# Performance work log

Measured on AMD Instinct MI355X. Metric: run time of the kernel, lower is better.

## Reference

```python
import jax, jax.numpy as jnp
import numpy as np

GEN_POLY = ("1011011", "1111001")  # constraint_length 7, rate 1/2
LARGE = 1e9  # metric for infeasible start states


def _build_trellis(gen_poly):
    """Static trellis tables (numpy, built at trace time).

    State = last mu input bits (most recent bit is MSB), matching the
    shift-register convention: next_state = [u, s_bits[:-1]].
    """
    conv_n = len(gen_poly)
    K = len(gen_poly[0])
    mu = K - 1
    ns, ni, no = 2 ** mu, 2, 2 ** conv_n
    g = np.array([[int(c) for c in p] for p in gen_poly])  # (conv_n, K)
    to_nodes = np.zeros((ns, ni), np.int32)
    op = np.zeros((ns, ni), np.int32)
    for s in range(ns):
        s_bits = [(s >> (mu - 1 - i)) & 1 for i in range(mu)]
        for u in range(ni):
            reg = np.array([u] + s_bits)          # [u_t, u_{t-1}, ..., u_{t-mu}]
            outs = (g @ reg) % 2                  # conv_n output bits
            op[s, u] = int("".join(map(str, outs)), 2)
            to_nodes[s, u] = int("".join(map(str, [u] + s_bits[:-1])), 2)
    from_nodes = np.zeros((ns, ni), np.int32)
    op_by_tonode = np.zeros((ns, ni), np.int32)
    cnt = np.zeros(ns, np.int32)
    for s in range(ns):
        for u in range(ni):
            t = to_nodes[s, u]
            from_nodes[t, cnt[t]] = s
            op_by_tonode[t, cnt[t]] = op[s, u]
            cnt[t] += 1
    op_bits = np.array([[(o >> (conv_n - 1 - j)) & 1 for j in range(conv_n)]
                        for o in range(no)], np.float32)  # (no, conv_n)
    return conv_n, ns, ni, to_nodes, from_nodes, op_by_tonode, op_bits


def setup_inputs() -> dict:
    key = jax.random.key(0)
    # noisy channel LLRs for B=512 codewords of length n=4096
    inputs = jax.random.normal(key, (512, 4096), dtype=jnp.float32) * 2.0
    return {"inputs": inputs}


def reference(inputs):
    conv_n, ns, ni, to_nodes_np, from_nodes_np, op_by_tonode_np, op_bits = \
        _build_trellis(GEN_POLY)
    tn = jnp.asarray(to_nodes_np)       # (ns, ni) next state
    fn = jnp.asarray(from_nodes_np)     # (ns, ni) predecessor states
    opt = jnp.asarray(op_by_tonode_np)  # (ns, ni) output symbol on that branch

    B, n = inputs.shape
    T = n // conv_n                     # number of trellis steps / info bits
    y = inputs.reshape(B, T, conv_n)

    # soft_llr branch metrics: bm[t,b,o] = sum_c y[b,t,c] * (1 - 2*op_bit[o,c])
    sign = jnp.asarray(1.0 - 2.0 * op_bits)          # (no, conv_n)
    bm = jnp.einsum('btc,oc->tbo', y, sign)          # (T, B, no)

    cum0 = jnp.full((B, ns), LARGE, jnp.float32).at[:, 0].set(0.0)
    st_rng = jnp.arange(ns)

    def acs(cum, bm_t):
        # add: metric of (prev_state i, output symbol j)
        sm = bm_t[:, None, :] + cum[:, :, None]      # (B, ns, no)
        # gather by to-node: candidates for each next state
        cand = sm[:, fn, opt]                        # (B, ns, ni)
        j = jnp.argmin(cand, axis=2)                 # compare-select
        tb = fn[st_rng[None, :], j]                  # traceback predecessor (B, ns)
        cum_t = jnp.min(cand, axis=2)
        return cum_t, (cum_t, tb)

    cum_T, (cms, tbs) = jax.lax.scan(acs, cum0, bm)  # tbs: (T, B, ns)

    # traceback from optimal terminal state
    term = jnp.argmin(cum_T, axis=1).astype(jnp.int32)

    def tb_step(st, tb_t):
        prev = jnp.take_along_axis(tb_t, st[:, None], axis=1)[:, 0]
        return prev, st

    p0, ys = jax.lax.scan(tb_step, term, tbs[1:], reverse=True)
    # path states at times 0..T (initial state is 0)
    paths = jnp.concatenate(
        [jnp.zeros((B, 1), jnp.int32), p0[:, None], jnp.swapaxes(ys, 0, 1)],
        axis=1)                                       # (B, T+1)

    # recover input bit per transition: bit u s.t. to_nodes[prev, u] == next
    match = tn[paths[:, :-1]] == paths[:, 1:][:, :, None]  # (B, T, ni)
    bits = jnp.sum(jnp.where(match, jnp.arange(ni, dtype=jnp.int32), 0), axis=-1)
    return bits.astype(jnp.float32)                   # (B, T) hard bit estimates
```

## Files before the change

kernel.cpp:

```cpp
#include <hip/hip_runtime.h>
#include <stdint.h>

#define T_STEPS 2048
#define NCHUNK  86
#define LARGEF  1.0e9f
typedef unsigned long long u64;
typedef unsigned uint2v __attribute__((ext_vector_type(2)));

__device__ __forceinline__ int par6(int x) { return __builtin_popcount((unsigned)x) & 1; }

constexpr int CARR[6] = {5, 6, 12, 8, 16, 32};

template<int CTRL>
__device__ __forceinline__ float xdpp(float x) {
  return __int_as_float(__builtin_amdgcn_update_dpp(0, __float_as_int(x), CTRL, 0xF, 0xF, true));
}
template<int CTRL>
__device__ __forceinline__ unsigned xdpp_u(unsigned x) {
  return (unsigned)__builtin_amdgcn_update_dpp(0, (int)x, CTRL, 0xF, 0xF, true);
}

__device__ __forceinline__ unsigned selmask_u(unsigned a_false, unsigned b_true, u64 m) {
  unsigned out;
  asm("v_cndmask_b32 %0, %1, %2, %3" : "=v"(out) : "v"(a_false), "v"(b_true), "s"(m));
  return out;
}

__device__ __forceinline__ unsigned exch16_u(unsigned x, u64 mrx) {
#if __has_builtin(__builtin_amdgcn_permlane16_swap)
  uint2v r = __builtin_amdgcn_permlane16_swap(x, x, false, false);
  return selmask_u(r.y, r.x, mrx);
#else
  (void)mrx;
  return (unsigned)__builtin_amdgcn_ds_swizzle((int)x, 0x401F);
#endif
}
__device__ __forceinline__ unsigned exch32_u(unsigned x, u64 mrx) {
#if __has_builtin(__builtin_amdgcn_permlane32_swap)
  uint2v r = __builtin_amdgcn_permlane32_swap(x, x, false, false);
  return selmask_u(r.y, r.x, mrx);
#else
  (void)mrx;
  return (unsigned)__shfl_xor((int)x, 32, 64);
#endif
}
__device__ __forceinline__ float exch16_f(float x, u64 mrx) {
  return __uint_as_float(exch16_u(__float_as_uint(x), mrx));
}
__device__ __forceinline__ float exch32_f(float x, u64 mrx) {
  return __uint_as_float(exch32_u(__float_as_uint(x), mrx));
}

struct Ctx {
  float sae[6], sbe[6];
  unsigned pdu[6];
  u64 pdm[6];
  u64 mrx16, mrx32;
};

template<int N>
__device__ __forceinline__ void bmcalc(const float4 (&fy)[12], float (&bm)[24], const Ctx& cx) {
#pragma unroll
  for (int k = 0; k < N; ++k) {
    const int ph = k % 6;
    const float y0 = (k & 1) ? fy[k >> 1].z : fy[k >> 1].x;
    const float y1 = (k & 1) ? fy[k >> 1].w : fy[k >> 1].y;
    bm[k] = fmaf(cx.sae[ph], y0, cx.sbe[ph] * y1);
  }
}

template<int N, int K>
__device__ __forceinline__ void fsteps(float& cum, unsigned& word,
                                       const float (&bm)[24], const Ctx& cx) {
  if constexpr (K < N) {
    constexpr int ph = K % 6;
    float ex; unsigned exw;
    if constexpr (ph == 0)      { ex = xdpp<0xB1>(cum);  exw = xdpp_u<0xB1>(word); }
    else if constexpr (ph == 1) { ex = xdpp<0x4E>(cum);  exw = xdpp_u<0x4E>(word); }
    else if constexpr (ph == 2) { ex = xdpp<0x141>(cum); exw = xdpp_u<0x141>(word); }
    else if constexpr (ph == 3) { ex = xdpp<0x140>(cum); exw = xdpp_u<0x140>(word); }
    else if constexpr (ph == 4) { ex = exch16_f(cum, cx.mrx16); exw = exch16_u(word, cx.mrx16); }
    else                        { ex = exch32_f(cum, cx.mrx32); exw = exch32_u(word, cx.mrx32); }
    const float cA = cum + bm[K];
    const float cB = ex - bm[K];
    const u64 b1 = __ballot(cB < cA);
    const u64 b2 = __ballot(cA < cB);
    const u64 tpm = (b1 & ~cx.pdm[ph]) | (cx.pdm[ph] & ~b2);
    word = selmask_u(word, exw, tpm) | (cx.pdu[ph] << (6 + K));
    cum = fminf(cA, cB);
    fsteps<N, K + 1>(cum, word, bm, cx);
  }
}

__global__ __launch_bounds__(64, 1) void viterbi_kernel(const float* __restrict__ in,
                                                        float* __restrict__ out) {
  __shared__ float y_lds[2 * T_STEPS];
  __shared__ unsigned tbf[NCHUNK * 64];

  const int b = blockIdx.x;
  const int lane = threadIdx.x;
  const float* yrow = in + (size_t)b * (2 * T_STEPS);

  {
    const float4* g = (const float4*)yrow;
    float4* l = (float4*)y_lds;
#pragma unroll
    for (int i = 0; i < 16; ++i) l[i * 64 + lane] = g[i * 64 + lane];
  }
  __syncthreads();

  Ctx cx;
#pragma unroll
  for (int ph = 0; ph < 6; ++ph) {
    const int pdv = par6(lane & CARR[ph]);
    int t = 0;
#pragma unroll
    for (int j = 0; j < 5; ++j) t |= par6(lane & CARR[(ph + 1 + j) % 6]) << j;
    t |= pdv << 5;
    const float sa = 1.0f - 2.0f * (float)par6(t & 45);
    const float sb = 1.0f - 2.0f * (float)par6(t & 60);
    cx.sae[ph] = pdv ? -sa : sa;
    cx.sbe[ph] = pdv ? -sb : sb;
    cx.pdu[ph] = (unsigned)pdv;
    cx.pdm[ph] = __ballot(pdv != 0);
  }
  {
    const u64 ODD16 = 0xFFFF0000FFFF0000ull;
    const u64 HI32  = 0xFFFFFFFF00000000ull;
#if __has_builtin(__builtin_amdgcn_permlane16_swap)
    uint2v p16 = __builtin_amdgcn_permlane16_swap((unsigned)lane, (unsigned)lane, false, false);
    const bool rxo = ((unsigned)__builtin_amdgcn_readlane((int)p16.x, 0) == 16u);
    cx.mrx16 = rxo ? ~ODD16 : ODD16;
#else
    cx.mrx16 = 0;
#endif
#if __has_builtin(__builtin_amdgcn_permlane32_swap)
    uint2v p32 = __builtin_amdgcn_permlane32_swap((unsigned)lane, (unsigned)lane, false, false);
    const bool rxh = ((unsigned)__builtin_amdgcn_readlane((int)p32.x, 0) == 32u);
    cx.mrx32 = rxh ? ~HI32 : HI32;
#else
    cx.mrx32 = 0;
#endif
  }

  float cum = (lane == 0) ? 0.0f : LARGEF;
  unsigned word = (unsigned)lane;
  float bm[24];
  float4 cur[12], nxt[12];
  const float4* y4 = (const float4*)y_lds;
#pragma unroll
  for (int j = 0; j < 12; ++j) cur[j] = y4[j];
  for (int cc = 0; cc < 42; ++cc) {
    const int c0 = 2 * cc;
    bmcalc<24>(cur, bm, cx);
#pragma unroll
    for (int j = 0; j < 12; ++j) nxt[j] = y4[12 * (c0 + 1) + j];
    fsteps<24, 0>(cum, word, bm, cx);
    tbf[c0 * 64 + lane] = word; word = (unsigned)lane;
    bmcalc<24>(nxt, bm, cx);
#pragma unroll
    for (int j = 0; j < 12; ++j) cur[j] = y4[12 * (c0 + 2) + j];
    fsteps<24, 0>(cum, word, bm, cx);
    tbf[(c0 + 1) * 64 + lane] = word; word = (unsigned)lane;
  }
  bmcalc<24>(cur, bm, cx);
#pragma unroll
  for (int j = 0; j < 4; ++j) nxt[j] = y4[1020 + j];
  fsteps<24, 0>(cum, word, bm, cx);
  tbf[84 * 64 + lane] = word; word = (unsigned)lane;
  bmcalc<8>(nxt, bm, cx);
  fsteps<8, 0>(cum, word, bm, cx);
  tbf[85 * 64 + lane] = word;

  const int stf = par6(lane & 12) | (par6(lane & 8) << 1) | (par6(lane & 16) << 2) |
                  (par6(lane & 32) << 3) | (par6(lane & 5) << 4) | (par6(lane & 6) << 5);
  float v = cum; int bs = stf; int bl = lane;
#pragma unroll
  for (int off = 32; off >= 1; off >>= 1) {
    const float ov = __shfl_xor(v, off, 64);
    const int os = __shfl_xor(bs, off, 64);
    const int ol = __shfl_xor(bl, off, 64);
    if (ov < v || (ov == v && os < bs)) { v = ov; bs = os; bl = ol; }
  }
  int lam = __builtin_amdgcn_readfirstlane(bl);

  const size_t ob = (size_t)b * T_STEPS;
  unsigned row = tbf[85 * 64 + lane];
  for (int c = 85; c >= 0; --c) {
    unsigned nrow = 0;
    if (c > 0) nrow = tbf[(c - 1) * 64 + lane];
    const unsigned w = (unsigned)__builtin_amdgcn_readlane((int)row, lam);
    const int nb = (c == 85) ? 8 : 24;
    if (lane < nb) out[ob + c * 24 + lane] = (float)((w >> (6 + lane)) & 1u);
    lam = (int)(w & 63u);
    row = nrow;
  }
}

extern "C" void kernel_launch(void* const* d_in, const int* in_sizes, int n_in,
                              void* d_out, int out_size, void* d_ws, size_t ws_size,
                              hipStream_t stream) {
  const float* in = (const float*)d_in[0];
  float* out = (float*)d_out;
  (void)in_sizes; (void)n_in; (void)out_size; (void)d_ws; (void)ws_size;
  viterbi_kernel<<<dim3(512), dim3(64), 0, stream>>>(in, out);
}
```

Before: 74.79 us.

## Fuse pairs of Viterbi ACS steps into radix-4 rounds with combined exchanges

Replaces the per-step radix-2 add-compare-select with a radix-4 round that processes two trellis steps at once. Each lane gathers three partner metrics (two single exchanges and one combined exchange) and computes the two-step minimum directly, so the second step no longer waits on the first step's exchange. This shortens the serial dependency chain per pair of steps. In return each round needs more exchange, ballot and select instructions and more precomputed sign/mask registers.

```diff
diff --git a/kernel.cpp b/kernel.cpp
--- a/kernel.cpp
+++ b/kernel.cpp
@@ -10,6 +10,7 @@
 __device__ __forceinline__ int par6(int x) { return __builtin_popcount((unsigned)x) & 1; }
 
 constexpr int CARR[6] = {5, 6, 12, 8, 16, 32};
+constexpr int MARR[6] = {1, 2, 7, 15, 16, 32};
 
 template<int CTRL>
 __device__ __forceinline__ float xdpp(float x) {
@@ -52,43 +53,77 @@
 }
 
 struct Ctx {
-  float sae[6], sbe[6];
-  unsigned pdu[6];
-  u64 pdm[6];
+  float saeA[3], sbeA[3];
+  float saeA2[3], sbeA2[3];
+  float saeB[3], sbeB[3];
+  unsigned pq0[3], pq1[3];
+  u64 pdmA[3], pdmA2[3], pdmB[3];
   u64 mrx16, mrx32;
 };
 
-template<int N>
-__device__ __forceinline__ void bmcalc(const float4 (&fy)[12], float (&bm)[24], const Ctx& cx) {
-#pragma unroll
-  for (int k = 0; k < N; ++k) {
-    const int ph = k % 6;
-    const float y0 = (k & 1) ? fy[k >> 1].z : fy[k >> 1].x;
-    const float y1 = (k & 1) ? fy[k >> 1].w : fy[k >> 1].y;
-    bm[k] = fmaf(cx.sae[ph], y0, cx.sbe[ph] * y1);
-  }
-}
-
-template<int N, int K>
-__device__ __forceinline__ void fsteps(float& cum, unsigned& word,
-                                       const float (&bm)[24], const Ctx& cx) {
-  if constexpr (K < N) {
-    constexpr int ph = K % 6;
-    float ex; unsigned exw;
-    if constexpr (ph == 0)      { ex = xdpp<0xB1>(cum);  exw = xdpp_u<0xB1>(word); }
-    else if constexpr (ph == 1) { ex = xdpp<0x4E>(cum);  exw = xdpp_u<0x4E>(word); }
-    else if constexpr (ph == 2) { ex = xdpp<0x141>(cum); exw = xdpp_u<0x141>(word); }
-    else if constexpr (ph == 3) { ex = xdpp<0x140>(cum); exw = xdpp_u<0x140>(word); }
-    else if constexpr (ph == 4) { ex = exch16_f(cum, cx.mrx16); exw = exch16_u(word, cx.mrx16); }
-    else                        { ex = exch32_f(cum, cx.mrx32); exw = exch32_u(word, cx.mrx32); }
-    const float cA = cum + bm[K];
-    const float cB = ex - bm[K];
-    const u64 b1 = __ballot(cB < cA);
-    const u64 b2 = __ballot(cA < cB);
-    const u64 tpm = (b1 & ~cx.pdm[ph]) | (cx.pdm[ph] & ~b2);
-    word = selmask_u(word, exw, tpm) | (cx.pdu[ph] << (6 + K));
-    cum = fminf(cA, cB);
-    fsteps<N, K + 1>(cum, word, bm, cx);
+__device__ __forceinline__ void mk(int ph, int l, float& sae, float& sbe, int& pd) {
+  const int pdv = par6(l & CARR[ph]);
+  int t = 0;
+#pragma unroll
+  for (int j = 0; j < 5; ++j) t |= par6(l & CARR[(ph + 1 + j) % 6]) << j;
+  t |= pdv << 5;
+  const float sa = 1.0f - 2.0f * (float)par6(t & 45);
+  const float sb = 1.0f - 2.0f * (float)par6(t & 60);
+  sae = pdv ? -sa : sa;
+  sbe = pdv ? -sb : sb;
+  pd = pdv;
+}
+
+template<int NR>
+__device__ __forceinline__ void bmcalc3(const float4 (&fy)[12], float (&bmA)[12],
+                                        float (&bmA2)[12], float (&bmB)[12], const Ctx& cx) {
+#pragma unroll
+  for (int r = 0; r < NR; ++r) {
+    const int rp = r % 3;
+    bmA[r]  = fmaf(cx.saeA[rp],  fy[r].x, cx.sbeA[rp]  * fy[r].y);
+    bmA2[r] = fmaf(cx.saeA2[rp], fy[r].x, cx.sbeA2[rp] * fy[r].y);
+    bmB[r]  = fmaf(cx.saeB[rp],  fy[r].z, cx.sbeB[rp]  * fy[r].w);
+  }
+}
+
+template<int NR, int R>
+__device__ __forceinline__ void frounds(float& cum, unsigned& word,
+                                        const float (&bmA)[12], const float (&bmA2)[12],
+                                        const float (&bmB)[12], const Ctx& cx) {
+  if constexpr (R < NR) {
+    constexpr int RP = R % 3;
+    float exA, exB_, exAB; unsigned wxA, wxB, wxAB;
+    if constexpr (RP == 0) {
+      exA  = xdpp<0xB1>(cum);  exB_ = xdpp<0x4E>(cum);  exAB = xdpp<0x1B>(cum);
+      wxA  = xdpp_u<0xB1>(word); wxB = xdpp_u<0x4E>(word); wxAB = xdpp_u<0x1B>(word);
+    } else if constexpr (RP == 1) {
+      exA  = xdpp<0x141>(cum); exB_ = xdpp<0x140>(cum); exAB = xdpp<0x128>(cum);
+      wxA  = xdpp_u<0x141>(word); wxB = xdpp_u<0x140>(word); wxAB = xdpp_u<0x128>(word);
+    } else {
+      exA  = exch16_f(cum, cx.mrx16);  exB_ = exch32_f(cum, cx.mrx32);
+      exAB = exch16_f(exB_, cx.mrx16);
+      wxA  = exch16_u(word, cx.mrx16); wxB  = exch32_u(word, cx.mrx32);
+      wxAB = exch16_u(wxB, cx.mrx16);
+    }
+    const float c00p = cum  + bmA[R];
+    const float c01p = exA  - bmA[R];
+    const float c10p = exB_ + bmA2[R];
+    const float c11p = exAB - bmA2[R];
+    const float u = fminf(c00p, c01p);
+    const float v = fminf(c10p, c11p);
+    const float x  = u + bmB[R];
+    const float yv = v - bmB[R];
+    cum = fminf(x, yv);
+    const u64 a1 = __ballot(c01p < c00p), a2 = __ballot(c00p < c01p);
+    const u64 o1 = __ballot(c11p < c10p), o2 = __ballot(c10p < c11p);
+    const u64 f1 = __ballot(yv < x),      f2 = __ballot(x < yv);
+    const u64 dA  = (a1 & ~cx.pdmA[RP])  | (cx.pdmA[RP]  & ~a2);
+    const u64 dAo = (o1 & ~cx.pdmA2[RP]) | (cx.pdmA2[RP] & ~o2);
+    const u64 dB  = (f1 & ~cx.pdmB[RP])  | (cx.pdmB[RP]  & ~f2);
+    const unsigned wu = selmask_u(word, wxA, dA)  | (cx.pq0[RP] << (6 + 2 * R));
+    const unsigned wv = selmask_u(wxB, wxAB, dAo) | (cx.pq1[RP] << (6 + 2 * R));
+    word = selmask_u(wu, wv, dB);
+    frounds<NR, R + 1>(cum, word, bmA, bmA2, bmB, cx);
   }
 }
 
@@ -111,18 +146,18 @@
 
   Ctx cx;
 #pragma unroll
-  for (int ph = 0; ph < 6; ++ph) {
-    const int pdv = par6(lane & CARR[ph]);
-    int t = 0;
-#pragma unroll
-    for (int j = 0; j < 5; ++j) t |= par6(lane & CARR[(ph + 1 + j) % 6]) << j;
-    t |= pdv << 5;
-    const float sa = 1.0f - 2.0f * (float)par6(t & 45);
-    const float sb = 1.0f - 2.0f * (float)par6(t & 60);
-    cx.sae[ph] = pdv ? -sa : sa;
-    cx.sbe[ph] = pdv ? -sb : sb;
-    cx.pdu[ph] = (unsigned)pdv;
-    cx.pdm[ph] = __ballot(pdv != 0);
+  for (int rp = 0; rp < 3; ++rp) {
+    const int pA = 2 * rp, pB = 2 * rp + 1;
+    const int mB = MARR[pB];
+    float sa, sb; int pd;
+    mk(pA, lane, sa, sb, pd);        cx.saeA[rp] = sa;  cx.sbeA[rp] = sb;  const int pdA = pd;
+    mk(pA, lane ^ mB, sa, sb, pd);   cx.saeA2[rp] = sa; cx.sbeA2[rp] = sb; const int pdA2 = pd;
+    mk(pB, lane, sa, sb, pd);        cx.saeB[rp] = sa;  cx.sbeB[rp] = sb;  const int pdB = pd;
+    cx.pq0[rp] = (unsigned)(pdA  | (pdB << 1));
+    cx.pq1[rp] = (unsigned)(pdA2 | (pdB << 1));
+    cx.pdmA[rp]  = __ballot(pdA != 0);
+    cx.pdmA2[rp] = __ballot(pdA2 != 0);
+    cx.pdmB[rp]  = __ballot(pdB != 0);
   }
   {
     const u64 ODD16 = 0xFFFF0000FFFF0000ull;
@@ -145,31 +180,31 @@
 
   float cum = (lane == 0) ? 0.0f : LARGEF;
   unsigned word = (unsigned)lane;
-  float bm[24];
+  float bmA[12], bmA2[12], bmB[12];
   float4 cur[12], nxt[12];
   const float4* y4 = (const float4*)y_lds;
 #pragma unroll
   for (int j = 0; j < 12; ++j) cur[j] = y4[j];
   for (int cc = 0; cc < 42; ++cc) {
     const int c0 = 2 * cc;
-    bmcalc<24>(cur, bm, cx);
+    bmcalc3<12>(cur, bmA, bmA2, bmB, cx);
 #pragma unroll
     for (int j = 0; j < 12; ++j) nxt[j] = y4[12 * (c0 + 1) + j];
-    fsteps<24, 0>(cum, word, bm, cx);
+    frounds<12, 0>(cum, word, bmA, bmA2, bmB, cx);
     tbf[c0 * 64 + lane] = word; word = (unsigned)lane;
-    bmcalc<24>(nxt, bm, cx);
+    bmcalc3<12>(nxt, bmA, bmA2, bmB, cx);
 #pragma unroll
     for (int j = 0; j < 12; ++j) cur[j] = y4[12 * (c0 + 2) + j];
-    fsteps<24, 0>(cum, word, bm, cx);
+    frounds<12, 0>(cum, word, bmA, bmA2, bmB, cx);
     tbf[(c0 + 1) * 64 + lane] = word; word = (unsigned)lane;
   }
-  bmcalc<24>(cur, bm, cx);
+  bmcalc3<12>(cur, bmA, bmA2, bmB, cx);
 #pragma unroll
   for (int j = 0; j < 4; ++j) nxt[j] = y4[1020 + j];
-  fsteps<24, 0>(cum, word, bm, cx);
+  frounds<12, 0>(cum, word, bmA, bmA2, bmB, cx);
   tbf[84 * 64 + lane] = word; word = (unsigned)lane;
-  bmcalc<8>(nxt, bm, cx);
-  fsteps<8, 0>(cum, word, bm, cx);
+  bmcalc3<4>(nxt, bmA, bmA2, bmB, cx);
+  frounds<4, 0>(cum, word, bmA, bmA2, bmB, cx);
   tbf[85 * 64 + lane] = word;
 
   const int stf = par6(lane & 12) | (par6(lane & 8) << 1) | (par6(lane & 16) << 2) |
```

After: 105.1 us. +40.6%, slower.

## Split Viterbi into ACS wave and helper wave for branch metrics and traceback words

Applied to the files above, without the earlier changes.

The block grows to two wavefronts. Wave 0 runs only the add-compare-select recursion and records one decision bit per step via an inline-asm xor/cmp/addc sequence. Wave 1 precomputes branch metrics into a triple-buffered LDS ring and rebuilds the survivor traceback words from those decision bits one chunk behind. This shortens the serial critical path of the ACS wave by moving the metric FMAs, word exchanges and selects off it. In exchange it adds a block-wide barrier every chunk (about 86 in total) and extra LDS traffic, and the barrier cost could offset the shorter per-step chain.

```diff
diff --git a/kernel.cpp b/kernel.cpp
--- a/kernel.cpp
+++ b/kernel.cpp
@@ -19,13 +19,11 @@
 __device__ __forceinline__ unsigned xdpp_u(unsigned x) {
   return (unsigned)__builtin_amdgcn_update_dpp(0, (int)x, CTRL, 0xF, 0xF, true);
 }
-
 __device__ __forceinline__ unsigned selmask_u(unsigned a_false, unsigned b_true, u64 m) {
   unsigned out;
   asm("v_cndmask_b32 %0, %1, %2, %3" : "=v"(out) : "v"(a_false), "v"(b_true), "s"(m));
   return out;
 }
-
 __device__ __forceinline__ unsigned exch16_u(unsigned x, u64 mrx) {
 #if __has_builtin(__builtin_amdgcn_permlane16_swap)
   uint2v r = __builtin_amdgcn_permlane16_swap(x, x, false, false);
@@ -44,72 +42,113 @@
   return (unsigned)__shfl_xor((int)x, 32, 64);
 #endif
 }
-__device__ __forceinline__ float exch16_f(float x, u64 mrx) {
-  return __uint_as_float(exch16_u(__float_as_uint(x), mrx));
-}
-__device__ __forceinline__ float exch32_f(float x, u64 mrx) {
-  return __uint_as_float(exch32_u(__float_as_uint(x), mrx));
-}
-
-struct Ctx {
-  float sae[6], sbe[6];
-  unsigned pdu[6];
-  u64 pdm[6];
-  u64 mrx16, mrx32;
-};
-
-template<int N>
-__device__ __forceinline__ void bmcalc(const float4 (&fy)[12], float (&bm)[24], const Ctx& cx) {
-#pragma unroll
-  for (int k = 0; k < N; ++k) {
-    const int ph = k % 6;
-    const float y0 = (k & 1) ? fy[k >> 1].z : fy[k >> 1].x;
-    const float y1 = (k & 1) ? fy[k >> 1].w : fy[k >> 1].y;
-    bm[k] = fmaf(cx.sae[ph], y0, cx.sbe[ph] * y1);
-  }
+template<int PH>
+__device__ __forceinline__ float exchf(float x, const u64 (&mrx)[2]) {
+  if constexpr (PH == 0) return xdpp<0xB1>(x);
+  else if constexpr (PH == 1) return xdpp<0x4E>(x);
+  else if constexpr (PH == 2) return xdpp<0x141>(x);
+  else if constexpr (PH == 3) return xdpp<0x140>(x);
+  else if constexpr (PH == 4) return __uint_as_float(exch16_u(__float_as_uint(x), mrx[0]));
+  else return __uint_as_float(exch32_u(__float_as_uint(x), mrx[1]));
+}
+template<int PH>
+__device__ __forceinline__ unsigned exchu(unsigned x, const u64 (&mrx)[2]) {
+  if constexpr (PH == 0) return xdpp_u<0xB1>(x);
+  else if constexpr (PH == 1) return xdpp_u<0x4E>(x);
+  else if constexpr (PH == 2) return xdpp_u<0x141>(x);
+  else if constexpr (PH == 3) return xdpp_u<0x140>(x);
+  else if constexpr (PH == 4) return exch16_u(x, mrx[0]);
+  else return exch32_u(x, mrx[1]);
+}
+
+template<int K>
+__device__ __forceinline__ float getbm(const float4 (&bk)[6]) {
+  constexpr int j = K >> 2;
+  if constexpr ((K & 3) == 0) return bk[j].x;
+  else if constexpr ((K & 3) == 1) return bk[j].y;
+  else if constexpr ((K & 3) == 2) return bk[j].z;
+  else return bk[j].w;
 }
 
 template<int N, int K>
-__device__ __forceinline__ void fsteps(float& cum, unsigned& word,
-                                       const float (&bm)[24], const Ctx& cx) {
+__device__ __forceinline__ void acsr(float& cum, unsigned& dw, const float4 (&bk)[6],
+                                     const unsigned (&sgn)[6], const u64 (&mrx)[2]) {
   if constexpr (K < N) {
     constexpr int ph = K % 6;
-    float ex; unsigned exw;
-    if constexpr (ph == 0)      { ex = xdpp<0xB1>(cum);  exw = xdpp_u<0xB1>(word); }
-    else if constexpr (ph == 1) { ex = xdpp<0x4E>(cum);  exw = xdpp_u<0x4E>(word); }
-    else if constexpr (ph == 2) { ex = xdpp<0x141>(cum); exw = xdpp_u<0x141>(word); }
-    else if constexpr (ph == 3) { ex = xdpp<0x140>(cum); exw = xdpp_u<0x140>(word); }
-    else if constexpr (ph == 4) { ex = exch16_f(cum, cx.mrx16); exw = exch16_u(word, cx.mrx16); }
-    else                        { ex = exch32_f(cum, cx.mrx32); exw = exch32_u(word, cx.mrx32); }
-    const float cA = cum + bm[K];
-    const float cB = ex - bm[K];
-    const u64 b1 = __ballot(cB < cA);
-    const u64 b2 = __ballot(cA < cB);
-    const u64 tpm = (b1 & ~cx.pdm[ph]) | (cx.pdm[ph] & ~b2);
-    word = selmask_u(word, exw, tpm) | (cx.pdu[ph] << (6 + K));
+    const float bmk = getbm<K>(bk);
+    const float ex = exchf<ph>(cum, mrx);
+    const float cA = cum + bmk;
+    const float cB = ex - bmk;
+    const float D = cA - cB;
     cum = fminf(cA, cB);
-    fsteps<N, K + 1>(cum, word, bm, cx);
-  }
-}
-
-__global__ __launch_bounds__(64, 1) void viterbi_kernel(const float* __restrict__ in,
-                                                        float* __restrict__ out) {
+    unsigned tmp;
+    asm("v_xor_b32 %0, %2, %3\n\t"
+        "v_cmp_gt_f32 vcc, 0, %0\n\t"
+        "v_addc_co_u32 %1, vcc, %1, %1, vcc"
+        : "=&v"(tmp), "+v"(dw)
+        : "v"(D), "v"(sgn[ph]) : "vcc");
+    acsr<N, K + 1>(cum, dw, bk, sgn, mrx);
+  }
+}
+
+template<int N, int K>
+__device__ __forceinline__ void wrec(unsigned& word, unsigned& dws, const unsigned (&pdu)[6],
+                                     const u64 (&pdm)[6], const u64 (&mrx)[2]) {
+  if constexpr (K < N) {
+    constexpr int ph = K % 6;
+    const unsigned exw = exchu<ph>(word, mrx);
+    asm("v_cmp_gt_i32 vcc, 0, %1\n\t"
+        "v_add_u32 %1, %1, %1\n\t"
+        "s_xor_b64 vcc, vcc, %3\n\t"
+        "v_cndmask_b32 %0, %0, %2, vcc"
+        : "+v"(word), "+v"(dws)
+        : "v"(exw), "s"(pdm[ph]) : "vcc");
+    word |= pdu[ph] << (6 + K);
+    wrec<N, K + 1>(word, dws, pdu, pdm, mrx);
+  }
+}
+
+template<int N>
+__device__ __forceinline__ void bmw(const float* ych, float* dst,
+                                    const float (&sae)[6], const float (&sbe)[6]) {
+  const float4* y4 = (const float4*)ych;
+  float4* d4 = (float4*)dst;
+#pragma unroll
+  for (int j = 0; j < N / 4; ++j) {
+    const float4 qa = y4[2 * j];
+    const float4 qb = y4[2 * j + 1];
+    float4 r;
+    r.x = fmaf(sae[(4 * j + 0) % 6], qa.x, sbe[(4 * j + 0) % 6] * qa.y);
+    r.y = fmaf(sae[(4 * j + 1) % 6], qa.z, sbe[(4 * j + 1) % 6] * qa.w);
+    r.z = fmaf(sae[(4 * j + 2) % 6], qb.x, sbe[(4 * j + 2) % 6] * qb.y);
+    r.w = fmaf(sae[(4 * j + 3) % 6], qb.z, sbe[(4 * j + 3) % 6] * qb.w);
+    d4[j] = r;
+  }
+}
+
+__global__ __launch_bounds__(128, 1) void viterbi_kernel(const float* __restrict__ in,
+                                                         float* __restrict__ out) {
   __shared__ float y_lds[2 * T_STEPS];
-  __shared__ unsigned tbf[NCHUNK * 64];
-
+  __shared__ float bmld[3][64][24];
+  __shared__ unsigned dwld[2][64];
+  __shared__ unsigned tbf[NCHUNK][64];
+  __shared__ int lam_sh;
+
+  const int tid = threadIdx.x;
+  const int lane = tid & 63;
+  const int w = tid >> 6;
   const int b = blockIdx.x;
-  const int lane = threadIdx.x;
-  const float* yrow = in + (size_t)b * (2 * T_STEPS);
 
   {
-    const float4* g = (const float4*)yrow;
+    const float4* g = (const float4*)(in + (size_t)b * (2 * T_STEPS));
     float4* l = (float4*)y_lds;
 #pragma unroll
-    for (int i = 0; i < 16; ++i) l[i * 64 + lane] = g[i * 64 + lane];
-  }
-  __syncthreads();
-
-  Ctx cx;
+    for (int i = 0; i < 8; ++i) l[i * 128 + tid] = g[i * 128 + tid];
+  }
+
+  float sae[6], sbe[6];
+  unsigned pdu[6], sgn[6];
+  u64 pdm[6], mrx[2];
 #pragma unroll
   for (int ph = 0; ph < 6; ++ph) {
     const int pdv = par6(lane & CARR[ph]);
@@ -119,81 +158,136 @@
     t |= pdv << 5;
     const float sa = 1.0f - 2.0f * (float)par6(t & 45);
     const float sb = 1.0f - 2.0f * (float)par6(t & 60);
-    cx.sae[ph] = pdv ? -sa : sa;
-    cx.sbe[ph] = pdv ? -sb : sb;
-    cx.pdu[ph] = (unsigned)pdv;
-    cx.pdm[ph] = __ballot(pdv != 0);
+    sae[ph] = pdv ? -sa : sa;
+    sbe[ph] = pdv ? -sb : sb;
+    pdu[ph] = (unsigned)pdv;
+    sgn[ph] = pdv ? 0u : 0x80000000u;
+    pdm[ph] = __ballot(pdv != 0);
   }
   {
     const u64 ODD16 = 0xFFFF0000FFFF0000ull;
-    const u64 HI32  = 0xFFFFFFFF00000000ull;
+    const u64 HI32 = 0xFFFFFFFF00000000ull;
 #if __has_builtin(__builtin_amdgcn_permlane16_swap)
     uint2v p16 = __builtin_amdgcn_permlane16_swap((unsigned)lane, (unsigned)lane, false, false);
-    const bool rxo = ((unsigned)__builtin_amdgcn_readlane((int)p16.x, 0) == 16u);
-    cx.mrx16 = rxo ? ~ODD16 : ODD16;
+    mrx[0] = (((unsigned)__builtin_amdgcn_readlane((int)p16.x, 0) == 16u)) ? ~ODD16 : ODD16;
 #else
-    cx.mrx16 = 0;
+    mrx[0] = 0;
 #endif
 #if __has_builtin(__builtin_amdgcn_permlane32_swap)
     uint2v p32 = __builtin_amdgcn_permlane32_swap((unsigned)lane, (unsigned)lane, false, false);
-    const bool rxh = ((unsigned)__builtin_amdgcn_readlane((int)p32.x, 0) == 32u);
-    cx.mrx32 = rxh ? ~HI32 : HI32;
+    mrx[1] = (((unsigned)__builtin_amdgcn_readlane((int)p32.x, 0) == 32u)) ? ~HI32 : HI32;
 #else
-    cx.mrx32 = 0;
+    mrx[1] = 0;
 #endif
   }
+  __syncthreads();
+
+  if (w == 1) {
+    bmw<24>(y_lds + 0, &bmld[0][lane][0], sae, sbe);
+    bmw<24>(y_lds + 48, &bmld[1][lane][0], sae, sbe);
+  }
+  __syncthreads();
 
   float cum = (lane == 0) ? 0.0f : LARGEF;
-  unsigned word = (unsigned)lane;
-  float bm[24];
-  float4 cur[12], nxt[12];
-  const float4* y4 = (const float4*)y_lds;
-#pragma unroll
-  for (int j = 0; j < 12; ++j) cur[j] = y4[j];
-  for (int cc = 0; cc < 42; ++cc) {
-    const int c0 = 2 * cc;
-    bmcalc<24>(cur, bm, cx);
-#pragma unroll
-    for (int j = 0; j < 12; ++j) nxt[j] = y4[12 * (c0 + 1) + j];
-    fsteps<24, 0>(cum, word, bm, cx);
-    tbf[c0 * 64 + lane] = word; word = (unsigned)lane;
-    bmcalc<24>(nxt, bm, cx);
-#pragma unroll
-    for (int j = 0; j < 12; ++j) cur[j] = y4[12 * (c0 + 2) + j];
-    fsteps<24, 0>(cum, word, bm, cx);
-    tbf[(c0 + 1) * 64 + lane] = word; word = (unsigned)lane;
-  }
-  bmcalc<24>(cur, bm, cx);
-#pragma unroll
-  for (int j = 0; j < 4; ++j) nxt[j] = y4[1020 + j];
-  fsteps<24, 0>(cum, word, bm, cx);
-  tbf[84 * 64 + lane] = word; word = (unsigned)lane;
-  bmcalc<8>(nxt, bm, cx);
-  fsteps<8, 0>(cum, word, bm, cx);
-  tbf[85 * 64 + lane] = word;
-
-  const int stf = par6(lane & 12) | (par6(lane & 8) << 1) | (par6(lane & 16) << 2) |
-                  (par6(lane & 32) << 3) | (par6(lane & 5) << 4) | (par6(lane & 6) << 5);
-  float v = cum; int bs = stf; int bl = lane;
-#pragma unroll
-  for (int off = 32; off >= 1; off >>= 1) {
-    const float ov = __shfl_xor(v, off, 64);
-    const int os = __shfl_xor(bs, off, 64);
-    const int ol = __shfl_xor(bl, off, 64);
-    if (ov < v || (ov == v && os < bs)) { v = ov; bs = os; bl = ol; }
-  }
-  int lam = __builtin_amdgcn_readfirstlane(bl);
-
-  const size_t ob = (size_t)b * T_STEPS;
-  unsigned row = tbf[85 * 64 + lane];
-  for (int c = 85; c >= 0; --c) {
-    unsigned nrow = 0;
-    if (c > 0) nrow = tbf[(c - 1) * 64 + lane];
-    const unsigned w = (unsigned)__builtin_amdgcn_readlane((int)row, lam);
-    const int nb = (c == 85) ? 8 : 24;
-    if (lane < nb) out[ob + c * 24 + lane] = (float)((w >> (6 + lane)) & 1u);
-    lam = (int)(w & 63u);
-    row = nrow;
+  unsigned dw = 0;
+  float4 bk0[6], bk1[6];
+  if (w == 0) {
+    const float4* p = (const float4*)&bmld[0][lane][0];
+#pragma unroll
+    for (int j = 0; j < 6; ++j) bk0[j] = p[j];
+  }
+
+#define W0_BLOCK(J)                                                                     \
+  {                                                                                     \
+    const float4* p = (const float4*)&bmld[((J) + 1) % 3][lane][0];                     \
+    if constexpr (((J) & 1) == 0) {                                                     \
+      _Pragma("unroll") for (int j = 0; j < 6; ++j) bk1[j] = p[j];                      \
+      acsr<24, 0>(cum, dw, bk0, sgn, mrx);                                              \
+    } else {                                                                            \
+      _Pragma("unroll") for (int j = 0; j < 6; ++j) bk0[j] = p[j];                      \
+      acsr<24, 0>(cum, dw, bk1, sgn, mrx);                                              \
+    }                                                                                   \
+    dwld[(J) & 1][lane] = dw;                                                           \
+    dw = 0;                                                                             \
+  }
+#define W1_BLOCK(J)                                                                     \
+  {                                                                                     \
+    const int c2 = base + (J) + 2;                                                      \
+    if (c2 != 85) bmw<24>(y_lds + 48 * c2, &bmld[((J) + 2) % 3][lane][0], sae, sbe);    \
+    else          bmw<8>(y_lds + 48 * c2, &bmld[((J) + 2) % 3][lane][0], sae, sbe);     \
+    if (base + (J) >= 1) {                                                              \
+      unsigned dws = dwld[((J) + 1) & 1][lane] << 8;                                    \
+      unsigned word = (unsigned)lane;                                                   \
+      wrec<24, 0>(word, dws, pdu, pdm, mrx);                                            \
+      tbf[base + (J) - 1][lane] = word;                                                 \
+    }                                                                                   \
+  }
+#define ITER(J)                                                                         \
+  if (w == 0) W0_BLOCK(J) else W1_BLOCK(J)                                              \
+  __syncthreads();
+
+  for (int base = 0; base < 84; base += 6) {
+    ITER(0) ITER(1) ITER(2) ITER(3) ITER(4) ITER(5)
+  }
+
+  if (w == 0) {
+    const float4* p = (const float4*)&bmld[1][lane][0];
+#pragma unroll
+    for (int j = 0; j < 6; ++j) bk1[j] = p[j];
+    acsr<24, 0>(cum, dw, bk0, sgn, mrx);
+    dwld[0][lane] = dw;
+    dw = 0;
+  } else {
+    unsigned dws = dwld[1][lane] << 8;
+    unsigned word = (unsigned)lane;
+    wrec<24, 0>(word, dws, pdu, pdm, mrx);
+    tbf[83][lane] = word;
+  }
+  __syncthreads();
+  if (w == 0) {
+    acsr<8, 0>(cum, dw, bk1, sgn, mrx);
+    dwld[1][lane] = dw;
+  } else {
+    unsigned dws = dwld[0][lane] << 8;
+    unsigned word = (unsigned)lane;
+    wrec<24, 0>(word, dws, pdu, pdm, mrx);
+    tbf[84][lane] = word;
+  }
+  __syncthreads();
+
+  if (w == 0) {
+    const int stf = par6(lane & 12) | (par6(lane & 8) << 1) | (par6(lane & 16) << 2) |
+                    (par6(lane & 32) << 3) | (par6(lane & 5) << 4) | (par6(lane & 6) << 5);
+    float v = cum; int bs = stf; int bl = lane;
+#pragma unroll
+    for (int off = 32; off >= 1; off >>= 1) {
+      const float ov = __shfl_xor(v, off, 64);
+      const int os = __shfl_xor(bs, off, 64);
+      const int ol = __shfl_xor(bl, off, 64);
+      if (ov < v || (ov == v && os < bs)) { v = ov; bs = os; bl = ol; }
+    }
+    if (lane == 0) lam_sh = bl;
+  } else {
+    unsigned dws = dwld[1][lane] << 24;
+    unsigned word = (unsigned)lane;
+    wrec<8, 0>(word, dws, pdu, pdm, mrx);
+    tbf[85][lane] = word;
+  }
+  __syncthreads();
+
+  if (w == 1) {
+    const size_t ob = (size_t)b * T_STEPS;
+    int lam = __builtin_amdgcn_readfirstlane(lam_sh);
+    unsigned row = tbf[85][lane];
+    for (int c = 85; c >= 0; --c) {
+      unsigned nrow = 0;
+      if (c > 0) nrow = tbf[c - 1][lane];
+      const unsigned ww = (unsigned)__builtin_amdgcn_readlane((int)row, lam);
+      const int nb = (c == 85) ? 8 : 24;
+      if (lane < nb) out[ob + c * 24 + lane] = (float)((ww >> (6 + lane)) & 1u);
+      lam = (int)(ww & 63u);
+      row = nrow;
+    }
   }
 }
 
@@ -203,5 +297,5 @@
   const float* in = (const float*)d_in[0];
   float* out = (float*)d_out;
   (void)in_sizes; (void)n_in; (void)out_size; (void)d_ws; (void)ws_size;
-  viterbi_kernel<<<dim3(512), dim3(64), 0, stream>>>(in, out);
-}
+  viterbi_kernel<<<dim3(512), dim3(128), 0, stream>>>(in, out);
+}
```

New measurement: 90.21 us. 20.6% more time.

## Split Viterbi into forward decision-bit pass, parallel chunk traceback rebuild, and traceback kernels

Applied to the files above, without the earlier changes.

The forward ACS loop now records one compare decision bit per step, produced with a compact xor/cmp/addc asm sequence. The per-step exchange and select of traceback words is removed from the serial critical path. A separate massively parallel kernel rebuilds the per-chunk traceback words from these decision bits, and a third kernel does the final traceback. This trades a shorter serial forward chain for extra global-memory round trips, two additional kernel launches, and workspace use, with a single fused fallback kernel when the workspace is too small.

```diff
diff --git a/kernel.cpp b/kernel.cpp
--- a/kernel.cpp
+++ b/kernel.cpp
@@ -4,6 +4,7 @@
 #define T_STEPS 2048
 #define NCHUNK  86
 #define LARGEF  1.0e9f
+#define NB      512
 typedef unsigned long long u64;
 typedef unsigned uint2v __attribute__((ext_vector_type(2)));
 
@@ -19,13 +20,11 @@
 __device__ __forceinline__ unsigned xdpp_u(unsigned x) {
   return (unsigned)__builtin_amdgcn_update_dpp(0, (int)x, CTRL, 0xF, 0xF, true);
 }
-
 __device__ __forceinline__ unsigned selmask_u(unsigned a_false, unsigned b_true, u64 m) {
   unsigned out;
   asm("v_cndmask_b32 %0, %1, %2, %3" : "=v"(out) : "v"(a_false), "v"(b_true), "s"(m));
   return out;
 }
-
 __device__ __forceinline__ unsigned exch16_u(unsigned x, u64 mrx) {
 #if __has_builtin(__builtin_amdgcn_permlane16_swap)
   uint2v r = __builtin_amdgcn_permlane16_swap(x, x, false, false);
@@ -44,134 +43,118 @@
   return (unsigned)__shfl_xor((int)x, 32, 64);
 #endif
 }
-__device__ __forceinline__ float exch16_f(float x, u64 mrx) {
-  return __uint_as_float(exch16_u(__float_as_uint(x), mrx));
-}
-__device__ __forceinline__ float exch32_f(float x, u64 mrx) {
-  return __uint_as_float(exch32_u(__float_as_uint(x), mrx));
-}
-
-struct Ctx {
+template<int PH>
+__device__ __forceinline__ float exchf(float x, const u64 (&mrx)[2]) {
+  if constexpr (PH == 0) return xdpp<0xB1>(x);
+  else if constexpr (PH == 1) return xdpp<0x4E>(x);
+  else if constexpr (PH == 2) return xdpp<0x141>(x);
+  else if constexpr (PH == 3) return xdpp<0x140>(x);
+  else if constexpr (PH == 4) return __uint_as_float(exch16_u(__float_as_uint(x), mrx[0]));
+  else return __uint_as_float(exch32_u(__float_as_uint(x), mrx[1]));
+}
+template<int PH>
+__device__ __forceinline__ unsigned exchu(unsigned x, const u64 (&mrx)[2]) {
+  if constexpr (PH == 0) return xdpp_u<0xB1>(x);
+  else if constexpr (PH == 1) return xdpp_u<0x4E>(x);
+  else if constexpr (PH == 2) return xdpp_u<0x141>(x);
+  else if constexpr (PH == 3) return xdpp_u<0x140>(x);
+  else if constexpr (PH == 4) return exch16_u(x, mrx[0]);
+  else return exch32_u(x, mrx[1]);
+}
+
+struct Phc {
   float sae[6], sbe[6];
+  unsigned sgn[6];
   unsigned pdu[6];
   u64 pdm[6];
-  u64 mrx16, mrx32;
+  u64 mrx[2];
 };
 
+__device__ __forceinline__ void mkconsts(int lane, Phc& p) {
+#pragma unroll
+  for (int ph = 0; ph < 6; ++ph) {
+    const int pdv = par6(lane & CARR[ph]);
+    int t = 0;
+#pragma unroll
+    for (int j = 0; j < 5; ++j) t |= par6(lane & CARR[(ph + 1 + j) % 6]) << j;
+    t |= pdv << 5;
+    const float sa = 1.0f - 2.0f * (float)par6(t & 45);
+    const float sb = 1.0f - 2.0f * (float)par6(t & 60);
+    p.sae[ph] = pdv ? -sa : sa;
+    p.sbe[ph] = pdv ? -sb : sb;
+    p.sgn[ph] = pdv ? 0u : 0x80000000u;
+    p.pdu[ph] = (unsigned)pdv;
+    p.pdm[ph] = __ballot(pdv != 0);
+  }
+  const u64 ODD16 = 0xFFFF0000FFFF0000ull, HI32 = 0xFFFFFFFF00000000ull;
+#if __has_builtin(__builtin_amdgcn_permlane16_swap)
+  {
+    uint2v r = __builtin_amdgcn_permlane16_swap((unsigned)lane, (unsigned)lane, false, false);
+    p.mrx[0] = (((unsigned)__builtin_amdgcn_readlane((int)r.x, 0) == 16u)) ? ~ODD16 : ODD16;
+  }
+#else
+  p.mrx[0] = 0;
+#endif
+#if __has_builtin(__builtin_amdgcn_permlane32_swap)
+  {
+    uint2v r = __builtin_amdgcn_permlane32_swap((unsigned)lane, (unsigned)lane, false, false);
+    p.mrx[1] = (((unsigned)__builtin_amdgcn_readlane((int)r.x, 0) == 32u)) ? ~HI32 : HI32;
+  }
+#else
+  p.mrx[1] = 0;
+#endif
+}
+
 template<int N>
-__device__ __forceinline__ void bmcalc(const float4 (&fy)[12], float (&bm)[24], const Ctx& cx) {
+__device__ __forceinline__ void bmcalc(const float4 (&fy)[12], float (&bm)[24],
+                                       const float (&sae)[6], const float (&sbe)[6]) {
 #pragma unroll
   for (int k = 0; k < N; ++k) {
     const int ph = k % 6;
     const float y0 = (k & 1) ? fy[k >> 1].z : fy[k >> 1].x;
     const float y1 = (k & 1) ? fy[k >> 1].w : fy[k >> 1].y;
-    bm[k] = fmaf(cx.sae[ph], y0, cx.sbe[ph] * y1);
+    bm[k] = fmaf(sae[ph], y0, sbe[ph] * y1);
   }
 }
 
 template<int N, int K>
-__device__ __forceinline__ void fsteps(float& cum, unsigned& word,
-                                       const float (&bm)[24], const Ctx& cx) {
+__device__ __forceinline__ void acs(float& cum, unsigned& dw, const float (&bm)[24],
+                                    const unsigned (&sgn)[6], const u64 (&mrx)[2]) {
   if constexpr (K < N) {
     constexpr int ph = K % 6;
-    float ex; unsigned exw;
-    if constexpr (ph == 0)      { ex = xdpp<0xB1>(cum);  exw = xdpp_u<0xB1>(word); }
-    else if constexpr (ph == 1) { ex = xdpp<0x4E>(cum);  exw = xdpp_u<0x4E>(word); }
-    else if constexpr (ph == 2) { ex = xdpp<0x141>(cum); exw = xdpp_u<0x141>(word); }
-    else if constexpr (ph == 3) { ex = xdpp<0x140>(cum); exw = xdpp_u<0x140>(word); }
-    else if constexpr (ph == 4) { ex = exch16_f(cum, cx.mrx16); exw = exch16_u(word, cx.mrx16); }
-    else                        { ex = exch32_f(cum, cx.mrx32); exw = exch32_u(word, cx.mrx32); }
+    const float ex = exchf<ph>(cum, mrx);
     const float cA = cum + bm[K];
     const float cB = ex - bm[K];
-    const u64 b1 = __ballot(cB < cA);
-    const u64 b2 = __ballot(cA < cB);
-    const u64 tpm = (b1 & ~cx.pdm[ph]) | (cx.pdm[ph] & ~b2);
-    word = selmask_u(word, exw, tpm) | (cx.pdu[ph] << (6 + K));
+    const float D = cA - cB;
     cum = fminf(cA, cB);
-    fsteps<N, K + 1>(cum, word, bm, cx);
-  }
-}
-
-__global__ __launch_bounds__(64, 1) void viterbi_kernel(const float* __restrict__ in,
-                                                        float* __restrict__ out) {
-  __shared__ float y_lds[2 * T_STEPS];
-  __shared__ unsigned tbf[NCHUNK * 64];
-
-  const int b = blockIdx.x;
-  const int lane = threadIdx.x;
-  const float* yrow = in + (size_t)b * (2 * T_STEPS);
-
-  {
-    const float4* g = (const float4*)yrow;
-    float4* l = (float4*)y_lds;
-#pragma unroll
-    for (int i = 0; i < 16; ++i) l[i * 64 + lane] = g[i * 64 + lane];
-  }
-  __syncthreads();
-
-  Ctx cx;
-#pragma unroll
-  for (int ph = 0; ph < 6; ++ph) {
-    const int pdv = par6(lane & CARR[ph]);
-    int t = 0;
-#pragma unroll
-    for (int j = 0; j < 5; ++j) t |= par6(lane & CARR[(ph + 1 + j) % 6]) << j;
-    t |= pdv << 5;
-    const float sa = 1.0f - 2.0f * (float)par6(t & 45);
-    const float sb = 1.0f - 2.0f * (float)par6(t & 60);
-    cx.sae[ph] = pdv ? -sa : sa;
-    cx.sbe[ph] = pdv ? -sb : sb;
-    cx.pdu[ph] = (unsigned)pdv;
-    cx.pdm[ph] = __ballot(pdv != 0);
-  }
-  {
-    const u64 ODD16 = 0xFFFF0000FFFF0000ull;
-    const u64 HI32  = 0xFFFFFFFF00000000ull;
-#if __has_builtin(__builtin_amdgcn_permlane16_swap)
-    uint2v p16 = __builtin_amdgcn_permlane16_swap((unsigned)lane, (unsigned)lane, false, false);
-    const bool rxo = ((unsigned)__builtin_amdgcn_readlane((int)p16.x, 0) == 16u);
-    cx.mrx16 = rxo ? ~ODD16 : ODD16;
-#else
-    cx.mrx16 = 0;
-#endif
-#if __has_builtin(__builtin_amdgcn_permlane32_swap)
-    uint2v p32 = __builtin_amdgcn_permlane32_swap((unsigned)lane, (unsigned)lane, false, false);
-    const bool rxh = ((unsigned)__builtin_amdgcn_readlane((int)p32.x, 0) == 32u);
-    cx.mrx32 = rxh ? ~HI32 : HI32;
-#else
-    cx.mrx32 = 0;
-#endif
-  }
-
-  float cum = (lane == 0) ? 0.0f : LARGEF;
-  unsigned word = (unsigned)lane;
-  float bm[24];
-  float4 cur[12], nxt[12];
-  const float4* y4 = (const float4*)y_lds;
-#pragma unroll
-  for (int j = 0; j < 12; ++j) cur[j] = y4[j];
-  for (int cc = 0; cc < 42; ++cc) {
-    const int c0 = 2 * cc;
-    bmcalc<24>(cur, bm, cx);
-#pragma unroll
-    for (int j = 0; j < 12; ++j) nxt[j] = y4[12 * (c0 + 1) + j];
-    fsteps<24, 0>(cum, word, bm, cx);
-    tbf[c0 * 64 + lane] = word; word = (unsigned)lane;
-    bmcalc<24>(nxt, bm, cx);
-#pragma unroll
-    for (int j = 0; j < 12; ++j) cur[j] = y4[12 * (c0 + 2) + j];
-    fsteps<24, 0>(cum, word, bm, cx);
-    tbf[(c0 + 1) * 64 + lane] = word; word = (unsigned)lane;
-  }
-  bmcalc<24>(cur, bm, cx);
-#pragma unroll
-  for (int j = 0; j < 4; ++j) nxt[j] = y4[1020 + j];
-  fsteps<24, 0>(cum, word, bm, cx);
-  tbf[84 * 64 + lane] = word; word = (unsigned)lane;
-  bmcalc<8>(nxt, bm, cx);
-  fsteps<8, 0>(cum, word, bm, cx);
-  tbf[85 * 64 + lane] = word;
-
+    unsigned tmp;
+    asm("v_xor_b32 %0, %2, %3\n\t"
+        "v_cmp_gt_f32 vcc, 0, %0\n\t"
+        "v_addc_co_u32 %1, vcc, %1, %1, vcc"
+        : "=&v"(tmp), "+v"(dw)
+        : "v"(D), "v"(sgn[ph]) : "vcc");
+    acs<N, K + 1>(cum, dw, bm, sgn, mrx);
+  }
+}
+
+template<int N, int K>
+__device__ __forceinline__ void wrec(unsigned& word, unsigned& dws, const unsigned (&pdu)[6],
+                                     const u64 (&pdm)[6], const u64 (&mrx)[2]) {
+  if constexpr (K < N) {
+    constexpr int ph = K % 6;
+    const unsigned exw = exchu<ph>(word, mrx);
+    asm("v_cmp_gt_i32 vcc, 0, %1\n\t"
+        "v_add_u32 %1, %1, %1\n\t"
+        "s_xor_b64 vcc, vcc, %3\n\t"
+        "v_cndmask_b32 %0, %0, %2, vcc"
+        : "+v"(word), "+v"(dws)
+        : "v"(exw), "s"(pdm[ph]) : "vcc");
+    word |= pdu[ph] << (6 + K);
+    wrec<N, K + 1>(word, dws, pdu, pdm, mrx);
+  }
+}
+
+__device__ __forceinline__ int term_argmin(float cum, int lane) {
   const int stf = par6(lane & 12) | (par6(lane & 8) << 1) | (par6(lane & 16) << 2) |
                   (par6(lane & 32) << 3) | (par6(lane & 5) << 4) | (par6(lane & 6) << 5);
   float v = cum; int bs = stf; int bl = lane;
@@ -182,13 +165,169 @@
     const int ol = __shfl_xor(bl, off, 64);
     if (ov < v || (ov == v && os < bs)) { v = ov; bs = os; bl = ol; }
   }
-  int lam = __builtin_amdgcn_readfirstlane(bl);
-
+  return bl;
+}
+
+__global__ __launch_bounds__(64, 1) void vit_fwd(const float* __restrict__ in,
+                                                 unsigned* __restrict__ dwg,
+                                                 int* __restrict__ term) {
+  __shared__ float y_lds[2 * T_STEPS];
+  const int b = blockIdx.x;
+  const int lane = threadIdx.x;
+  {
+    const float4* g = (const float4*)(in + (size_t)b * (2 * T_STEPS));
+    float4* l = (float4*)y_lds;
+#pragma unroll
+    for (int i = 0; i < 16; ++i) l[i * 64 + lane] = g[i * 64 + lane];
+  }
+  __syncthreads();
+
+  Phc p;
+  mkconsts(lane, p);
+
+  float cum = (lane == 0) ? 0.0f : LARGEF;
+  float bm[24];
+  float4 cur[12], nxt[12];
+  const float4* y4 = (const float4*)y_lds;
+  unsigned* dwp = dwg + (size_t)b * (NCHUNK * 64) + lane;
+  unsigned dw;
+#pragma unroll
+  for (int j = 0; j < 12; ++j) cur[j] = y4[j];
+  for (int cc = 0; cc < 42; ++cc) {
+    const int c0 = 2 * cc;
+    bmcalc<24>(cur, bm, p.sae, p.sbe);
+#pragma unroll
+    for (int j = 0; j < 12; ++j) nxt[j] = y4[12 * (c0 + 1) + j];
+    dw = 0; acs<24, 0>(cum, dw, bm, p.sgn, p.mrx);
+    *dwp = dw; dwp += 64;
+    bmcalc<24>(nxt, bm, p.sae, p.sbe);
+#pragma unroll
+    for (int j = 0; j < 12; ++j) cur[j] = y4[12 * (c0 + 2) + j];
+    dw = 0; acs<24, 0>(cum, dw, bm, p.sgn, p.mrx);
+    *dwp = dw; dwp += 64;
+  }
+  bmcalc<24>(cur, bm, p.sae, p.sbe);
+#pragma unroll
+  for (int j = 0; j < 4; ++j) nxt[j] = y4[1020 + j];
+  dw = 0; acs<24, 0>(cum, dw, bm, p.sgn, p.mrx);
+  *dwp = dw; dwp += 64;
+  bmcalc<8>(nxt, bm, p.sae, p.sbe);
+  dw = 0; acs<8, 0>(cum, dw, bm, p.sgn, p.mrx);
+  *dwp = dw;
+
+  const int bl = term_argmin(cum, lane);
+  if (lane == 0) term[b] = bl;
+}
+
+__global__ __launch_bounds__(256, 1) void vit_rec(const unsigned* __restrict__ dwg,
+                                                  unsigned* __restrict__ tbfg) {
+  const int tid = threadIdx.x;
+  const int lane = tid & 63;
+  const int wv = tid >> 6;
+  const int idx = blockIdx.x * 4 + wv;
+  const unsigned ui = (unsigned)idx;
+  const int c = (int)(ui % (unsigned)NCHUNK);
+
+  Phc p;
+  mkconsts(lane, p);
+
+  const unsigned dw = dwg[(size_t)idx * 64 + lane];
+  unsigned word = (unsigned)lane;
+  if (c == NCHUNK - 1) {
+    unsigned dws = dw << 24;
+    wrec<8, 0>(word, dws, p.pdu, p.pdm, p.mrx);
+  } else {
+    unsigned dws = dw << 8;
+    wrec<24, 0>(word, dws, p.pdu, p.pdm, p.mrx);
+  }
+  tbfg[(size_t)idx * 64 + lane] = word;
+}
+
+__global__ __launch_bounds__(64, 1) void vit_tb(const unsigned* __restrict__ tbfg,
+                                                const int* __restrict__ term,
+                                                float* __restrict__ out) {
+  const int b = blockIdx.x;
+  const int lane = threadIdx.x;
+  unsigned rows[NCHUNK];
+  const unsigned* tp = tbfg + (size_t)b * (NCHUNK * 64) + lane;
+#pragma unroll
+  for (int c = 0; c < NCHUNK; ++c) rows[c] = tp[c * 64];
+  int lam = term[b];
   const size_t ob = (size_t)b * T_STEPS;
-  unsigned row = tbf[85 * 64 + lane];
+#pragma unroll
+  for (int cc = 0; cc < NCHUNK; ++cc) {
+    const int c = NCHUNK - 1 - cc;
+    const unsigned w = (unsigned)__builtin_amdgcn_readlane((int)rows[c], lam);
+    const int nb = (c == NCHUNK - 1) ? 8 : 24;
+    if (lane < nb) out[ob + c * 24 + lane] = (float)((w >> (6 + lane)) & 1u);
+    lam = (int)(w & 63u);
+  }
+}
+
+__global__ __launch_bounds__(64, 1) void vit_fb(const float* __restrict__ in,
+                                                float* __restrict__ out) {
+  __shared__ float y_lds[2 * T_STEPS];
+  __shared__ unsigned dwl[NCHUNK][64];
+  __shared__ unsigned tbf[NCHUNK][64];
+  const int b = blockIdx.x;
+  const int lane = threadIdx.x;
+  {
+    const float4* g = (const float4*)(in + (size_t)b * (2 * T_STEPS));
+    float4* l = (float4*)y_lds;
+#pragma unroll
+    for (int i = 0; i < 16; ++i) l[i * 64 + lane] = g[i * 64 + lane];
+  }
+  __syncthreads();
+  Phc p;
+  mkconsts(lane, p);
+  float cum = (lane == 0) ? 0.0f : LARGEF;
+  float bm[24];
+  float4 cur[12], nxt[12];
+  const float4* y4 = (const float4*)y_lds;
+  unsigned dw;
+#pragma unroll
+  for (int j = 0; j < 12; ++j) cur[j] = y4[j];
+  for (int cc = 0; cc < 42; ++cc) {
+    const int c0 = 2 * cc;
+    bmcalc<24>(cur, bm, p.sae, p.sbe);
+#pragma unroll
+    for (int j = 0; j < 12; ++j) nxt[j] = y4[12 * (c0 + 1) + j];
+    dw = 0; acs<24, 0>(cum, dw, bm, p.sgn, p.mrx);
+    dwl[c0][lane] = dw;
+    bmcalc<24>(nxt, bm, p.sae, p.sbe);
+#pragma unroll
+    for (int j = 0; j < 12; ++j) cur[j] = y4[12 * (c0 + 2) + j];
+    dw = 0; acs<24, 0>(cum, dw, bm, p.sgn, p.mrx);
+    dwl[c0 + 1][lane] = dw;
+  }
+  bmcalc<24>(cur, bm, p.sae, p.sbe);
+#pragma unroll
+  for (int j = 0; j < 4; ++j) nxt[j] = y4[1020 + j];
+  dw = 0; acs<24, 0>(cum, dw, bm, p.sgn, p.mrx);
+  dwl[84][lane] = dw;
+  bmcalc<8>(nxt, bm, p.sae, p.sbe);
+  dw = 0; acs<8, 0>(cum, dw, bm, p.sgn, p.mrx);
+  dwl[85][lane] = dw;
+
+  for (int c = 0; c < 85; ++c) {
+    unsigned dws = dwl[c][lane] << 8;
+    unsigned word = (unsigned)lane;
+    wrec<24, 0>(word, dws, p.pdu, p.pdm, p.mrx);
+    tbf[c][lane] = word;
+  }
+  {
+    unsigned dws = dwl[85][lane] << 24;
+    unsigned word = (unsigned)lane;
+    wrec<8, 0>(word, dws, p.pdu, p.pdm, p.mrx);
+    tbf[85][lane] = word;
+  }
+
+  int lam = __builtin_amdgcn_readfirstlane(term_argmin(cum, lane));
+  const size_t ob = (size_t)b * T_STEPS;
+  unsigned row = tbf[85][lane];
   for (int c = 85; c >= 0; --c) {
     unsigned nrow = 0;
-    if (c > 0) nrow = tbf[(c - 1) * 64 + lane];
+    if (c > 0) nrow = tbf[c - 1][lane];
     const unsigned w = (unsigned)__builtin_amdgcn_readlane((int)row, lam);
     const int nb = (c == 85) ? 8 : 24;
     if (lane < nb) out[ob + c * 24 + lane] = (float)((w >> (6 + lane)) & 1u);
@@ -202,6 +341,17 @@
                               hipStream_t stream) {
   const float* in = (const float*)d_in[0];
   float* out = (float*)d_out;
-  (void)in_sizes; (void)n_in; (void)out_size; (void)d_ws; (void)ws_size;
-  viterbi_kernel<<<dim3(512), dim3(64), 0, stream>>>(in, out);
-}
+  (void)in_sizes; (void)n_in; (void)out_size;
+  const size_t nwords = (size_t)NB * NCHUNK * 64;
+  const size_t need = nwords * 4 * 2 + NB * 4;
+  if (ws_size >= need) {
+    unsigned* dwg = (unsigned*)d_ws;
+    unsigned* tbfg = dwg + nwords;
+    int* term = (int*)(tbfg + nwords);
+    vit_fwd<<<dim3(NB), dim3(64), 0, stream>>>(in, dwg, term);
+    vit_rec<<<dim3((NB * NCHUNK) / 4), dim3(256), 0, stream>>>(dwg, tbfg);
+    vit_tb<<<dim3(NB), dim3(64), 0, stream>>>(tbfg, term, out);
+  } else {
+    vit_fb<<<dim3(NB), dim3(64), 0, stream>>>(in, out);
+  }
+}
```

After: 75.94 us. About the same (+1.5%).
